# Performance work log

Hardware: AMD Instinct MI355X
Metric: run time of the kernel (lower is better)

## Reference

```python
import jax, jax.numpy as jnp
import numpy as np


def setup_inputs() -> dict:
    key = jax.random.key(0)
    k1, k2 = jax.random.split(key)
    N, D, C = 65536, 512, 64
    embeddings = jax.random.normal(k1, (N, D), dtype=jnp.float32)
    labels = jax.random.randint(k2, (N,), 0, C, dtype=jnp.int64)
    return {"embeddings": embeddings, "labels": labels, "num_classes": C}


def reference(embeddings, labels, num_classes):
    # Per-class mean (prototypes) via segment reductions. Labels are assumed
    # to be 0..C-1 with all classes present, so unique(labels) == arange(C)
    # and local_labels == labels (faithful to the torch loop in that regime).
    ones = jnp.ones(labels.shape, dtype=embeddings.dtype)
    counts = jax.ops.segment_sum(ones, labels, num_segments=num_classes)  # [C]
    sums = jax.ops.segment_sum(embeddings, labels, num_segments=num_classes)  # [C, D]
    prototypes = sums / counts[:, None]

    # Euclidean cdist: ||e||^2 + ||p||^2 - 2 e.p^T, clamped for numerical safety
    e2 = jnp.sum(embeddings * embeddings, axis=1, keepdims=True)  # [N, 1]
    p2 = jnp.sum(prototypes * prototypes, axis=1)  # [C]
    cross = embeddings @ prototypes.T  # [N, C]
    d2 = jnp.maximum(e2 + p2[None, :] - 2.0 * cross, 1e-12)
    logits = -jnp.sqrt(d2)  # [N, C], negative distances

    log_probs = jax.nn.log_softmax(logits, axis=1)
    n = labels.shape[0]
    nll = -log_probs[jnp.arange(n), labels]
    loss = jnp.mean(nll)
    accuracy = jnp.mean((jnp.argmax(logits, axis=1) == labels).astype(jnp.float32))
    return (loss, accuracy)
```

## Files before the change

kernel.cpp:

```cpp
#include <hip/hip_runtime.h>
#include <math.h>

#define NROWS 65536
#define DIM   512
#define NCLS  64
#define CCAP  1280

typedef __attribute__((ext_vector_type(4))) float f32x4;
typedef __attribute__((ext_vector_type(8))) short s16x8;

#define WS_PROTOSUM 0
#define WS_CURSORS  32768
#define WS_LOSS     32832
#define WS_ACC      32833
#define WS_DONE     32834
#define WS_P2       32836
#define WS_PERM     32912
#define WS_PBF      114944
#define WS_E2G      131328
#define WS_EBF      196864
#define WS_EXT_BYTES 67896320ULL
#define MEMSET_WORDS 32835

static __device__ __forceinline__ unsigned short f2bf(float f) {
    unsigned int u = __float_as_uint(f);
    u += 0x7FFF + ((u >> 16) & 1);
    return (unsigned short)(u >> 16);
}
static __device__ __forceinline__ float bf2f(unsigned short h) {
    return __uint_as_float(((unsigned int)h) << 16);
}

__global__ __launch_bounds__(256) void k_scatter(const int* __restrict__ labels,
                                                 int* __restrict__ cursors,
                                                 int* __restrict__ perm) {
    __shared__ int lh[NCLS], lb[NCLS];
    int t = threadIdx.x;
    if (t < NCLS) lh[t] = 0;
    __syncthreads();
    int i = blockIdx.x * 256 + t;
    int lab = labels[i];
    int rank = atomicAdd(&lh[lab], 1);
    __syncthreads();
    if (t < NCLS) lb[t] = atomicAdd(&cursors[t], lh[t]);
    __syncthreads();
    int pos = lb[lab] + rank;
    if (pos < CCAP) perm[lab * CCAP + pos] = i;
}

__global__ __launch_bounds__(256) void k_psum(const float* __restrict__ emb,
                                              const int* __restrict__ cursors,
                                              const int* __restrict__ perm,
                                              float* __restrict__ protoSum) {
    __shared__ int permS[CCAP];
    __shared__ float4 red[256];
    int t   = threadIdx.x;
    int c   = blockIdx.x >> 5;
    int sub = blockIdx.x & 31;
    int dc  = sub & 3;
    int rs  = sub >> 2;
    int tl  = t & 31;
    int g   = t >> 5;

    int cnt = cursors[c];
    int n = (cnt < CCAP) ? cnt : CCAP;
    for (int i = t; i < n; i += 256) permS[i] = perm[c * CCAP + i];
    __syncthreads();

    const float4* eb = (const float4*)emb + dc * 32 + tl;
    float4 acc = make_float4(0.f, 0.f, 0.f, 0.f);
#pragma unroll 4
    for (int i = rs * 8 + g; i < n; i += 64) {
        int r = permS[i];
        float4 v = eb[(size_t)r * 128];
        acc.x += v.x; acc.y += v.y; acc.z += v.z; acc.w += v.w;
    }
    red[t] = acc;
    __syncthreads();
    if (t < 32) {
        float4 s = red[t];
#pragma unroll
        for (int gg = 1; gg < 8; ++gg) {
            float4 v = red[gg * 32 + t];
            s.x += v.x; s.y += v.y; s.z += v.z; s.w += v.w;
        }
        float* dst = &protoSum[(size_t)c * DIM + dc * 128 + t * 4];
        atomicAdd(dst + 0, s.x);
        atomicAdd(dst + 1, s.y);
        atomicAdd(dst + 2, s.z);
        atomicAdd(dst + 3, s.w);
    }
}

__global__ __launch_bounds__(512) void k_protofin(const float* __restrict__ protoSum,
                                                  const int* __restrict__ cursors,
                                                  unsigned short* __restrict__ pBf,
                                                  float* __restrict__ p2) {
    int c = blockIdx.x, d = threadIdx.x;
    float mean = protoSum[(size_t)c * DIM + d] / (float)cursors[c];
    unsigned short mb = f2bf(mean);
    int kc = d >> 5, quad = (d >> 3) & 3, j = d & 7;
    int nt = c >> 4, l15 = c & 15;
    pBf[(size_t)(((kc * 4 + quad) * 4 + nt) * 16 + l15) * 8 + j] = mb;
    float mf = bf2f(mb);
    float sq = mf * mf;
#pragma unroll
    for (int o = 32; o > 0; o >>= 1) sq += __shfl_down(sq, o, 64);
    __shared__ float red[8];
    if ((d & 63) == 0) red[d >> 6] = sq;
    __syncthreads();
    if (d == 0) {
        float ss = 0.f;
#pragma unroll
        for (int w = 0; w < 8; ++w) ss += red[w];
        p2[c] = ss;
    }
}

__global__ __launch_bounds__(256) void k_prep(const float* __restrict__ emb,
                                              unsigned short* __restrict__ ebf,
                                              float* __restrict__ e2g) {
    int t = threadIdx.x, lane = t & 63, wv = t >> 6;
    int wid = blockIdx.x * 4 + wv;
    for (int row = wid; row < NROWS; row += 8192) {
        const float4* rp = (const float4*)(emb + (size_t)row * DIM) + lane * 2;
        float4 v0 = rp[0];
        float4 v1 = rp[1];
        s16x8 h;
        h[0] = f2bf(v0.x); h[1] = f2bf(v0.y); h[2] = f2bf(v0.z); h[3] = f2bf(v0.w);
        h[4] = f2bf(v1.x); h[5] = f2bf(v1.y); h[6] = f2bf(v1.z); h[7] = f2bf(v1.w);
        *(s16x8*)(ebf + (size_t)row * DIM + lane * 8) = h;
        float sq = v0.x * v0.x + v0.y * v0.y + v0.z * v0.z + v0.w * v0.w
                 + v1.x * v1.x + v1.y * v1.y + v1.z * v1.z + v1.w * v1.w;
#pragma unroll
        for (int o = 1; o < 64; o <<= 1) sq += __shfl_xor(sq, o, 64);
        if (lane == 0) e2g[row] = sq;
    }
}

#define LROWS 64
#define LGRID (NROWS / LROWS)

__global__ __launch_bounds__(256, 4) void k_logits2(const unsigned short* __restrict__ ebf,
                                                 const float* __restrict__ e2g,
                                                 const int* __restrict__ labels,
                                                 const unsigned short* __restrict__ pBf,
                                                 const float* __restrict__ p2,
                                                 float* __restrict__ lossAcc,
                                                 float* __restrict__ accAcc,
                                                 unsigned int* __restrict__ doneCnt,
                                                 float* __restrict__ out) {
    __shared__ float rb[8];
    int t    = threadIdx.x;
    int lane = t & 63;
    int wv   = t >> 6;
    int quad = lane >> 4;
    int l15  = lane & 15;
    int rbase = blockIdx.x * LROWS;
    int row   = wv * 16 + l15;

    f32x4 acc[4];
#pragma unroll
    for (int nt = 0; nt < 4; ++nt) acc[nt] = (f32x4){0.f, 0.f, 0.f, 0.f};

    const s16x8* ap = (const s16x8*)(ebf + (size_t)(rbase + row) * DIM) + quad;
    const s16x8* bp = (const s16x8*)pBf + quad * 64 + l15;

#pragma unroll 4
    for (int kc = 0; kc < 16; ++kc) {
        s16x8 a = ap[kc * 4];
#pragma unroll
        for (int nt = 0; nt < 4; ++nt) {
            s16x8 b = bp[(size_t)kc * 256 + nt * 16];
            acc[nt] = __builtin_amdgcn_mfma_f32_16x16x32_bf16(a, b, acc[nt], 0, 0, 0);
        }
    }

    float nlls = 0.f, corr = 0.f;
#pragma unroll
    for (int reg = 0; reg < 4; ++reg) {
        int rloc = wv * 16 + quad * 4 + reg;
        float e2v = e2g[rbase + rloc];
        float lg[4];
#pragma unroll
        for (int nt = 0; nt < 4; ++nt) {
            float d2 = e2v + p2[nt * 16 + l15] - 2.f * acc[nt][reg];
            d2 = fmaxf(d2, 1e-12f);
            lg[nt] = -sqrtf(d2);
        }
        float mv = lg[0]; int mc = l15;
#pragma unroll
        for (int nt = 1; nt < 4; ++nt) {
            int cix = nt * 16 + l15;
            if (lg[nt] > mv) { mv = lg[nt]; mc = cix; }
        }
#pragma unroll
        for (int o = 1; o < 16; o <<= 1) {
            float mo = __shfl_xor(mv, o, 64);
            int   co = __shfl_xor(mc, o, 64);
            if (mo > mv || (mo == mv && co < mc)) { mv = mo; mc = co; }
        }
        int lab = labels[rbase + rloc];
        float se = 0.f, ll = 0.f;
#pragma unroll
        for (int nt = 0; nt < 4; ++nt) se += __expf(lg[nt] - mv);
        if ((lab & 15) == l15) ll = lg[lab >> 4];
#pragma unroll
        for (int o = 1; o < 16; o <<= 1) {
            se += __shfl_xor(se, o, 64);
            ll += __shfl_xor(ll, o, 64);
        }
        if (l15 == 0) {
            nlls += __logf(se) + mv - ll;
            corr += (mc == lab) ? 1.f : 0.f;
        }
    }
#pragma unroll
    for (int o = 1; o < 64; o <<= 1) {
        nlls += __shfl_xor(nlls, o, 64);
        corr += __shfl_xor(corr, o, 64);
    }
    if (lane == 0) { rb[wv] = nlls; rb[4 + wv] = corr; }
    __syncthreads();
    if (t == 0) {
        atomicAdd(lossAcc, rb[0] + rb[1] + rb[2] + rb[3]);
        atomicAdd(accAcc, rb[4] + rb[5] + rb[6] + rb[7]);
        __threadfence();
        unsigned int tk = atomicAdd(doneCnt, 1u);
        if (tk == LGRID - 1) {
            float ls  = atomicAdd(lossAcc, 0.f);
            float as_ = atomicAdd(accAcc, 0.f);
            out[0] = ls * (1.f / NROWS);
            out[1] = as_ * (1.f / NROWS);
        }
    }
}

__global__ __launch_bounds__(256) void k_logits(const float* __restrict__ emb,
                                                const int* __restrict__ labels,
                                                const unsigned short* __restrict__ pBf,
                                                const float* __restrict__ p2,
                                                float* __restrict__ lossAcc,
                                                float* __restrict__ accAcc,
                                                unsigned int* __restrict__ doneCnt,
                                                float* __restrict__ out) {
    __shared__ float e2s[LROWS];
    __shared__ float rb[8];

    int t    = threadIdx.x;
    int lane = t & 63;
    int wv   = t >> 6;
    int quad = lane >> 4;
    int l15  = lane & 15;
    int rbase = blockIdx.x * LROWS;
    int row   = wv * 16 + l15;

    f32x4 acc[4];
#pragma unroll
    for (int nt = 0; nt < 4; ++nt) acc[nt] = (f32x4){0.f, 0.f, 0.f, 0.f};
    float e2a = 0.f;

    const float4* rp = (const float4*)(emb + (size_t)(rbase + row) * DIM) + quad * 2;
    const s16x8*  bp = (const s16x8*)pBf + quad * 64 + l15;

#pragma unroll 4
    for (int kc = 0; kc < 16; ++kc) {
        float4 g0 = rp[kc * 8];
        float4 g1 = rp[kc * 8 + 1];
        e2a += g0.x * g0.x + g0.y * g0.y + g0.z * g0.z + g0.w * g0.w
             + g1.x * g1.x + g1.y * g1.y + g1.z * g1.z + g1.w * g1.w;
        s16x8 a;
        a[0] = f2bf(g0.x); a[1] = f2bf(g0.y); a[2] = f2bf(g0.z); a[3] = f2bf(g0.w);
        a[4] = f2bf(g1.x); a[5] = f2bf(g1.y); a[6] = f2bf(g1.z); a[7] = f2bf(g1.w);
#pragma unroll
        for (int nt = 0; nt < 4; ++nt) {
            s16x8 b = bp[(size_t)kc * 256 + nt * 16];
            acc[nt] = __builtin_amdgcn_mfma_f32_16x16x32_bf16(a, b, acc[nt], 0, 0, 0);
        }
    }

    e2a += __shfl_xor(e2a, 16, 64);
    e2a += __shfl_xor(e2a, 32, 64);
    if (quad == 0) e2s[row] = e2a;
    __syncthreads();

    float nlls = 0.f, corr = 0.f;
#pragma unroll
    for (int reg = 0; reg < 4; ++reg) {
        int rloc = wv * 16 + quad * 4 + reg;
        float e2v = e2s[rloc];
        float lg[4];
#pragma unroll
        for (int nt = 0; nt < 4; ++nt) {
            float d2 = e2v + p2[nt * 16 + l15] - 2.f * acc[nt][reg];
            d2 = fmaxf(d2, 1e-12f);
            lg[nt] = -sqrtf(d2);
        }
        float mv = lg[0]; int mc = l15;
#pragma unroll
        for (int nt = 1; nt < 4; ++nt) {
            int cix = nt * 16 + l15;
            if (lg[nt] > mv) { mv = lg[nt]; mc = cix; }
        }
#pragma unroll
        for (int o = 1; o < 16; o <<= 1) {
            float mo = __shfl_xor(mv, o, 64);
            int   co = __shfl_xor(mc, o, 64);
            if (mo > mv || (mo == mv && co < mc)) { mv = mo; mc = co; }
        }
        int lab = labels[rbase + rloc];
        float se = 0.f, ll = 0.f;
#pragma unroll
        for (int nt = 0; nt < 4; ++nt) se += __expf(lg[nt] - mv);
        if ((lab & 15) == l15) ll = lg[lab >> 4];
#pragma unroll
        for (int o = 1; o < 16; o <<= 1) {
            se += __shfl_xor(se, o, 64);
            ll += __shfl_xor(ll, o, 64);
        }
        if (l15 == 0) {
            nlls += __logf(se) + mv - ll;
            corr += (mc == lab) ? 1.f : 0.f;
        }
    }
#pragma unroll
    for (int o = 1; o < 64; o <<= 1) {
        nlls += __shfl_xor(nlls, o, 64);
        corr += __shfl_xor(corr, o, 64);
    }
    if (lane == 0) { rb[wv] = nlls; rb[4 + wv] = corr; }
    __syncthreads();
    if (t == 0) {
        atomicAdd(lossAcc, rb[0] + rb[1] + rb[2] + rb[3]);
        atomicAdd(accAcc, rb[4] + rb[5] + rb[6] + rb[7]);
        __threadfence();
        unsigned int tk = atomicAdd(doneCnt, 1u);
        if (tk == LGRID - 1) {
            float ls  = atomicAdd(lossAcc, 0.f);
            float as_ = atomicAdd(accAcc, 0.f);
            out[0] = ls * (1.f / NROWS);
            out[1] = as_ * (1.f / NROWS);
        }
    }
}

extern "C" void kernel_launch(void* const* d_in, const int* in_sizes, int n_in,
                              void* d_out, int out_size, void* d_ws, size_t ws_size,
                              hipStream_t stream) {
    const float* emb    = (const float*)d_in[0];
    const int*   labels = (const int*)d_in[1];
    float* out = (float*)d_out;

    float* wsf = (float*)d_ws;
    int*   wsi = (int*)d_ws;
    float*          protoSum = wsf + WS_PROTOSUM;
    int*            cursors  = wsi + WS_CURSORS;
    float*          lossAcc  = wsf + WS_LOSS;
    float*          accAcc   = wsf + WS_ACC;
    unsigned int*   doneCnt  = (unsigned int*)(wsi + WS_DONE);
    float*          p2       = wsf + WS_P2;
    int*            perm     = wsi + WS_PERM;
    unsigned short* pBf      = (unsigned short*)(wsf + WS_PBF);
    float*          e2g      = wsf + WS_E2G;
    unsigned short* ebf      = (unsigned short*)(wsf + WS_EBF);

    hipMemsetAsync(d_ws, 0, MEMSET_WORDS * sizeof(int), stream);

    k_scatter<<<NROWS / 256, 256, 0, stream>>>(labels, cursors, perm);
    if (ws_size >= WS_EXT_BYTES) {
        k_prep<<<2048, 256, 0, stream>>>(emb, ebf, e2g);
        k_psum<<<NCLS * 32, 256, 0, stream>>>(emb, cursors, perm, protoSum);
        k_protofin<<<NCLS, 512, 0, stream>>>(protoSum, cursors, pBf, p2);
        k_logits2<<<LGRID, 256, 0, stream>>>(ebf, e2g, labels, pBf, p2,
                                             lossAcc, accAcc, doneCnt, out);
    } else {
        k_psum<<<NCLS * 32, 256, 0, stream>>>(emb, cursors, perm, protoSum);
        k_protofin<<<NCLS, 512, 0, stream>>>(protoSum, cursors, pBf, p2);
        k_logits<<<LGRID, 256, 0, stream>>>(emb, labels, pBf, p2,
                                            lossAcc, accAcc, doneCnt, out);
    }
}
```

Measured before the change: 293.2 us.

## Fuse bf16 conversion and row-norm prep into per-class prototype sum kernel

Removes the separate k_prep pass and has the prototype-sum kernel, which already reads every embedding row through the class permutation, also write the bf16 copy and partial squared norms. Each of the four column chunks writes its own partial norm, and the logits kernel adds the four partials. This saves one full read of the 128MB fp32 embedding matrix and a kernel launch. In exchange the bf16 stores are scattered 8-byte writes in permutation order, the logits kernel makes four norm loads per row instead of one, and the workspace requirement grows. Rows beyond the per-class capacity would not be converted.

```diff
diff --git a/kernel.cpp b/kernel.cpp
--- a/kernel.cpp
+++ b/kernel.cpp
@@ -17,9 +17,9 @@
 #define WS_P2       32836
 #define WS_PERM     32912
 #define WS_PBF      114944
-#define WS_E2G      131328
-#define WS_EBF      196864
-#define WS_EXT_BYTES 67896320ULL
+#define WS_E2P      131328
+#define WS_EBF      393472
+#define WS_EXT_BYTES 68682752ULL
 #define MEMSET_WORDS 32835
 
 static __device__ __forceinline__ unsigned short f2bf(float f) {
@@ -46,6 +46,60 @@
     __syncthreads();
     int pos = lb[lab] + rank;
     if (pos < CCAP) perm[lab * CCAP + pos] = i;
+}
+
+__global__ __launch_bounds__(256) void k_psumprep(const float* __restrict__ emb,
+                                                  const int* __restrict__ cursors,
+                                                  const int* __restrict__ perm,
+                                                  float* __restrict__ protoSum,
+                                                  unsigned short* __restrict__ ebf,
+                                                  float* __restrict__ e2p) {
+    __shared__ int permS[CCAP];
+    __shared__ float4 red[256];
+    int t   = threadIdx.x;
+    int c   = blockIdx.x >> 5;
+    int sub = blockIdx.x & 31;
+    int dc  = sub & 3;
+    int rs  = sub >> 2;
+    int tl  = t & 31;
+    int g   = t >> 5;
+
+    int cnt = cursors[c];
+    int n = (cnt < CCAP) ? cnt : CCAP;
+    for (int i = t; i < n; i += 256) permS[i] = perm[c * CCAP + i];
+    __syncthreads();
+
+    const float4* eb = (const float4*)emb + dc * 32 + tl;
+    float* e2o = e2p + (size_t)dc * NROWS;
+    float4 acc = make_float4(0.f, 0.f, 0.f, 0.f);
+#pragma unroll 2
+    for (int i = rs * 8 + g; i < n; i += 64) {
+        int r = permS[i];
+        float4 v = eb[(size_t)r * 128];
+        acc.x += v.x; acc.y += v.y; acc.z += v.z; acc.w += v.w;
+        ushort4 h;
+        h.x = f2bf(v.x); h.y = f2bf(v.y); h.z = f2bf(v.z); h.w = f2bf(v.w);
+        *(ushort4*)(ebf + (size_t)r * DIM + dc * 128 + tl * 4) = h;
+        float sq = v.x * v.x + v.y * v.y + v.z * v.z + v.w * v.w;
+#pragma unroll
+        for (int o = 1; o < 32; o <<= 1) sq += __shfl_xor(sq, o, 64);
+        if (tl == 0) e2o[r] = sq;
+    }
+    red[t] = acc;
+    __syncthreads();
+    if (t < 32) {
+        float4 s = red[t];
+#pragma unroll
+        for (int gg = 1; gg < 8; ++gg) {
+            float4 v = red[gg * 32 + t];
+            s.x += v.x; s.y += v.y; s.z += v.z; s.w += v.w;
+        }
+        float* dst = &protoSum[(size_t)c * DIM + dc * 128 + t * 4];
+        atomicAdd(dst + 0, s.x);
+        atomicAdd(dst + 1, s.y);
+        atomicAdd(dst + 2, s.z);
+        atomicAdd(dst + 3, s.w);
+    }
 }
 
 __global__ __launch_bounds__(256) void k_psum(const float* __restrict__ emb,
@@ -117,32 +171,11 @@
     }
 }
 
-__global__ __launch_bounds__(256) void k_prep(const float* __restrict__ emb,
-                                              unsigned short* __restrict__ ebf,
-                                              float* __restrict__ e2g) {
-    int t = threadIdx.x, lane = t & 63, wv = t >> 6;
-    int wid = blockIdx.x * 4 + wv;
-    for (int row = wid; row < NROWS; row += 8192) {
-        const float4* rp = (const float4*)(emb + (size_t)row * DIM) + lane * 2;
-        float4 v0 = rp[0];
-        float4 v1 = rp[1];
-        s16x8 h;
-        h[0] = f2bf(v0.x); h[1] = f2bf(v0.y); h[2] = f2bf(v0.z); h[3] = f2bf(v0.w);
-        h[4] = f2bf(v1.x); h[5] = f2bf(v1.y); h[6] = f2bf(v1.z); h[7] = f2bf(v1.w);
-        *(s16x8*)(ebf + (size_t)row * DIM + lane * 8) = h;
-        float sq = v0.x * v0.x + v0.y * v0.y + v0.z * v0.z + v0.w * v0.w
-                 + v1.x * v1.x + v1.y * v1.y + v1.z * v1.z + v1.w * v1.w;
-#pragma unroll
-        for (int o = 1; o < 64; o <<= 1) sq += __shfl_xor(sq, o, 64);
-        if (lane == 0) e2g[row] = sq;
-    }
-}
-
 #define LROWS 64
 #define LGRID (NROWS / LROWS)
 
 __global__ __launch_bounds__(256, 4) void k_logits2(const unsigned short* __restrict__ ebf,
-                                                 const float* __restrict__ e2g,
+                                                 const float* __restrict__ e2p,
                                                  const int* __restrict__ labels,
                                                  const unsigned short* __restrict__ pBf,
                                                  const float* __restrict__ p2,
@@ -180,7 +213,9 @@
 #pragma unroll
     for (int reg = 0; reg < 4; ++reg) {
         int rloc = wv * 16 + quad * 4 + reg;
-        float e2v = e2g[rbase + rloc];
+        int grow = rbase + rloc;
+        float e2v = e2p[grow] + e2p[NROWS + grow]
+                  + e2p[2 * NROWS + grow] + e2p[3 * NROWS + grow];
         float lg[4];
 #pragma unroll
         for (int nt = 0; nt < 4; ++nt) {
@@ -200,7 +235,7 @@
             int   co = __shfl_xor(mc, o, 64);
             if (mo > mv || (mo == mv && co < mc)) { mv = mo; mc = co; }
         }
-        int lab = labels[rbase + rloc];
+        int lab = labels[grow];
         float se = 0.f, ll = 0.f;
 #pragma unroll
         for (int nt = 0; nt < 4; ++nt) se += __expf(lg[nt] - mv);
@@ -361,17 +396,17 @@
     float*          p2       = wsf + WS_P2;
     int*            perm     = wsi + WS_PERM;
     unsigned short* pBf      = (unsigned short*)(wsf + WS_PBF);
-    float*          e2g      = wsf + WS_E2G;
+    float*          e2p      = wsf + WS_E2P;
     unsigned short* ebf      = (unsigned short*)(wsf + WS_EBF);
 
     hipMemsetAsync(d_ws, 0, MEMSET_WORDS * sizeof(int), stream);
 
     k_scatter<<<NROWS / 256, 256, 0, stream>>>(labels, cursors, perm);
     if (ws_size >= WS_EXT_BYTES) {
-        k_prep<<<2048, 256, 0, stream>>>(emb, ebf, e2g);
-        k_psum<<<NCLS * 32, 256, 0, stream>>>(emb, cursors, perm, protoSum);
+        k_psumprep<<<NCLS * 32, 256, 0, stream>>>(emb, cursors, perm, protoSum,
+                                                  ebf, e2p);
         k_protofin<<<NCLS, 512, 0, stream>>>(protoSum, cursors, pBf, p2);
-        k_logits2<<<LGRID, 256, 0, stream>>>(ebf, e2g, labels, pBf, p2,
+        k_logits2<<<LGRID, 256, 0, stream>>>(ebf, e2p, labels, pBf, p2,
                                              lossAcc, accAcc, doneCnt, out);
     } else {
         k_psum<<<NCLS * 32, 256, 0, stream>>>(emb, cursors, perm, protoSum);
```

Result: faster. 279.5 us (-4.7%).
